# Kernel optimization log

Measured on AMD Instinct MI355X. Metric: run time of the kernel, lower is better.

## Reference

```python
import jax, jax.numpy as jnp
import numpy as np

B = 8388608  # batch

def moth(x, a, b):
    # per-feature parametric elementwise activation: a * x * sigmoid(b * x)
    return a * x * jax.nn.sigmoid(b * x)

def setup_inputs() -> dict:
    key = jax.random.key(0)
    ks = jax.random.split(key, 12)
    inp = {
        'x':  jax.random.normal(ks[0], (B, 2), dtype=jnp.float32),
        'W1': jax.random.normal(ks[1], (2, 8), dtype=jnp.float32) * (1.0 / np.sqrt(2)),
        'b1': jax.random.normal(ks[2], (8,), dtype=jnp.float32) * 0.01,
        'a1': jax.random.normal(ks[3], (8,), dtype=jnp.float32) * 0.1 + 1.0,
        'c1': jax.random.normal(ks[4], (8,), dtype=jnp.float32) * 0.1 + 1.0,
        'W2': jax.random.normal(ks[5], (8, 4), dtype=jnp.float32) * (1.0 / np.sqrt(8)),
        'b2': jax.random.normal(ks[6], (4,), dtype=jnp.float32) * 0.01,
        'a2': jax.random.normal(ks[7], (4,), dtype=jnp.float32) * 0.1 + 1.0,
        'c2': jax.random.normal(ks[8], (4,), dtype=jnp.float32) * 0.1 + 1.0,
        'W3': jax.random.normal(ks[9], (4, 1), dtype=jnp.float32) * (1.0 / np.sqrt(4)),
        'b3': jax.random.normal(ks[10], (1,), dtype=jnp.float32) * 0.01,
    }
    return inp

def reference(x, W1, b1, a1, c1, W2, b2, a2, c2, W3, b3):
    h = x @ W1 + b1            # [B, 8]
    h = moth(h, a1, c1)        # [B, 8]
    h = h @ W2 + b2            # [B, 4]
    h = moth(h, a2, c2)        # [B, 4]
    out = h @ W3 + b3          # [B, 1]
    return out
```

## Files before the change

kernel.cpp:

```cpp
#include <hip/hip_runtime.h>

#define NLOG2E -1.44269504088896340736f

typedef float f32x2 __attribute__((ext_vector_type(2)));


__global__ void prefold_kernel(
    const float* __restrict__ W1, const float* __restrict__ b1,
    const float* __restrict__ a1, const float* __restrict__ c1,
    const float* __restrict__ W2, const float* __restrict__ b2,
    const float* __restrict__ a2, const float* __restrict__ c2,
    const float* __restrict__ W3, const float* __restrict__ b3,
    float* __restrict__ C)
{
    if (threadIdx.x == 0 && blockIdx.x == 0) {
        for (int j = 0; j < 8; ++j) {
            float ncl = c1[j] * NLOG2E;
            C[j]      = W1[j]     * ncl;
            C[8 + j]  = W1[8 + j] * ncl;
            C[16 + j] = b1[j]     * ncl;
            float k1 = a1[j] / ncl;
            for (int k = 0; k < 4; ++k)
                C[24 + j * 4 + k] = W2[j * 4 + k] * k1;
        }
        for (int k = 0; k < 4; ++k) {
            C[56 + k] = b2[k];
            C[60 + k] = c2[k] * NLOG2E;
            C[64 + k] = a2[k] * W3[k];
        }
        C[68] = b3[0];
    }
}

__device__ __forceinline__ f32x2 moth2(float4 p, const f32x2* __restrict__ Cp,
                                       float bb3)
{
    f32x2 u[2][4];
#pragma unroll
    for (int r = 0; r < 2; ++r) {
        float X0 = r ? p.z : p.x;
        float X1 = r ? p.w : p.y;
        f32x2 x0b = {X0, X0};
        f32x2 x1b = {X1, X1};
#pragma unroll
        for (int pj = 0; pj < 4; ++pj)
            u[r][pj] = __builtin_elementwise_fma(
                           x0b, Cp[pj],
                           __builtin_elementwise_fma(x1b, Cp[4 + pj],
                                                     Cp[8 + pj]));
    }

#pragma unroll
    for (int r = 0; r < 2; ++r)
#pragma unroll
        for (int pj = 0; pj < 4; ++pj) {
            f32x2 e;
            e[0] = __builtin_amdgcn_exp2f(u[r][pj][0]);
            e[1] = __builtin_amdgcn_exp2f(u[r][pj][1]);
            f32x2 d = e + 1.0f;
            f32x2 s;
            s[0] = __builtin_amdgcn_rcpf(d[0]);
            s[1] = __builtin_amdgcn_rcpf(d[1]);
            u[r][pj] *= s;
        }

    f32x2 res;
#pragma unroll
    for (int r = 0; r < 2; ++r) {
        f32x2 ta = Cp[28], tb = Cp[29];
#pragma unroll
        for (int j = 0; j < 8; ++j) {
            float hj = u[r][j >> 1][j & 1];
            f32x2 hb = {hj, hj};
            ta = __builtin_elementwise_fma(hb, Cp[12 + j * 2 + 0], ta);
            tb = __builtin_elementwise_fma(hb, Cp[12 + j * 2 + 1], tb);
        }
        f32x2 u2a = Cp[30] * ta;
        f32x2 u2b = Cp[31] * tb;
        f32x2 ea, eb;
        ea[0] = __builtin_amdgcn_exp2f(u2a[0]);
        ea[1] = __builtin_amdgcn_exp2f(u2a[1]);
        eb[0] = __builtin_amdgcn_exp2f(u2b[0]);
        eb[1] = __builtin_amdgcn_exp2f(u2b[1]);
        f32x2 da = ea + 1.0f, db = eb + 1.0f;
        f32x2 sa, sb;
        sa[0] = __builtin_amdgcn_rcpf(da[0]);
        sa[1] = __builtin_amdgcn_rcpf(da[1]);
        sb[0] = __builtin_amdgcn_rcpf(db[0]);
        sb[1] = __builtin_amdgcn_rcpf(db[1]);
        f32x2 pa = ta * sa;
        f32x2 pb = tb * sb;
        f32x2 acc = {bb3, 0.0f};
        acc = __builtin_elementwise_fma(pa, Cp[32], acc);
        acc = __builtin_elementwise_fma(pb, Cp[33], acc);
        res[r] = acc[0] + acc[1];
    }
    return res;
}

__global__ __launch_bounds__(256, 6) void PlaygroundModel_66365834658304_kernel(
    const float* __restrict__ x, const float* __restrict__ C,
    float* __restrict__ out, int rows)
{
    const f32x2* Cp = (const f32x2*)C;
    float bb3 = C[68];

    long long n4f    = (long long)rows >> 1;
    long long g      = (long long)blockIdx.x * blockDim.x + threadIdx.x;
    long long stride = (long long)gridDim.x * blockDim.x;

    const float4* x4 = (const float4*)x;
    f32x2* o2 = (f32x2*)out;

    long long idx = g;
    if (idx < n4f) {
        float4 p = x4[idx];
        for (;;) {
            long long nidx = idx + stride;
            bool has = (nidx < n4f);
            float4 np;
            if (has) np = x4[nidx];
            o2[idx] = moth2(p, Cp, bb3);
            if (!has) break;
            p = np;
            idx = nidx;
        }
    }

    if (g == 0 && (rows & 1)) {
        const float* uw0  = C;
        const float* uw1  = C + 8;
        const float* ub   = C + 16;
        const float* w2f  = C + 24;
        const float* bb2  = C + 56;
        const float* ncl2 = C + 60;
        const float* aw2  = C + 64;
        long long rr = (long long)rows - 1;
        float x0 = x[rr * 2 + 0], x1 = x[rr * 2 + 1];
        float h[8];
#pragma unroll
        for (int j = 0; j < 8; ++j) {
            float uu = fmaf(x0, uw0[j], fmaf(x1, uw1[j], ub[j]));
            float s  = __builtin_amdgcn_rcpf(
                           1.0f + __builtin_amdgcn_exp2f(uu));
            h[j] = uu * s;
        }
        float o = bb3;
#pragma unroll
        for (int kk = 0; kk < 4; ++kk) {
            float t = bb2[kk];
#pragma unroll
            for (int j = 0; j < 8; ++j) t = fmaf(h[j], w2f[j * 4 + kk], t);
            float u2 = ncl2[kk] * t;
            float sg = __builtin_amdgcn_rcpf(
                           1.0f + __builtin_amdgcn_exp2f(u2));
            o = fmaf(t * sg, aw2[kk], o);
        }
        out[rr] = o;
    }
}

extern "C" void kernel_launch(void* const* d_in, const int* in_sizes, int n_in,
                              void* d_out, int out_size, void* d_ws, size_t ws_size,
                              hipStream_t stream) {
    const float* x  = (const float*)d_in[0];
    const float* W1 = (const float*)d_in[1];
    const float* b1 = (const float*)d_in[2];
    const float* a1 = (const float*)d_in[3];
    const float* c1 = (const float*)d_in[4];
    const float* W2 = (const float*)d_in[5];
    const float* b2 = (const float*)d_in[6];
    const float* a2 = (const float*)d_in[7];
    const float* c2 = (const float*)d_in[8];
    const float* W3 = (const float*)d_in[9];
    const float* b3 = (const float*)d_in[10];
    float* out = (float*)d_out;
    float* C   = (float*)d_ws;

    prefold_kernel<<<1, 64, 0, stream>>>(W1, b1, a1, c1, W2, b2, a2, c2,
                                         W3, b3, C);

    int rows = in_sizes[0] / 2;
    long long n4 = (long long)rows >> 1;

    int block = 256;
    long long want = (n4 + (long long)block * 4 - 1) / ((long long)block * 4);
    int grid = (int)(want < 1 ? 1 : (want > 4096 ? 4096 : want));

    PlaygroundModel_66365834658304_kernel<<<grid, block, 0, stream>>>(
        x, C, out, rows);
}
```

Measured before the change: 129.7 us.

## Deepen load prefetch to two iterations, use 32-bit indices, shrink grid

The grid-stride loop now keeps two float4 loads in flight ahead of compute, using clamped unconditional loads instead of a guarded single prefetch. Index arithmetic moves from 64-bit to 32-bit to cut scalar and address instructions. The grid is capped at 1536 blocks instead of 4096, so each thread runs more iterations. The clamped loads add a few redundant reads at the tail, and the smaller grid may lower occupancy and the latency hiding it provides.

```diff
diff --git a/kernel.cpp b/kernel.cpp
--- a/kernel.cpp
+++ b/kernel.cpp
@@ -105,25 +105,28 @@
     const f32x2* Cp = (const f32x2*)C;
     float bb3 = C[68];
 
-    long long n4f    = (long long)rows >> 1;
-    long long g      = (long long)blockIdx.x * blockDim.x + threadIdx.x;
-    long long stride = (long long)gridDim.x * blockDim.x;
+    int n4   = rows >> 1;
+    int n4m1 = n4 - 1;
+    int T    = (int)(gridDim.x * blockDim.x);
+    int g    = (int)(blockIdx.x * blockDim.x + threadIdx.x);
 
     const float4* x4 = (const float4*)x;
     f32x2* o2 = (f32x2*)out;
 
-    long long idx = g;
-    if (idx < n4f) {
-        float4 p = x4[idx];
-        for (;;) {
-            long long nidx = idx + stride;
-            bool has = (nidx < n4f);
-            float4 np;
-            if (has) np = x4[nidx];
-            o2[idx] = moth2(p, Cp, bb3);
-            if (!has) break;
-            p = np;
-            idx = nidx;
+    if (g < n4) {
+        int i0 = g;
+        int i1 = (i0 + T <= n4m1) ? i0 + T : n4m1;
+        float4 A = x4[i0];
+        float4 B = x4[i1];
+        int idx = i0, nxt = i0 + T;
+        while (true) {
+            int nn = nxt + T;
+            int ld = (nn <= n4m1) ? nn : n4m1;
+            float4 Cq = x4[ld];
+            o2[idx] = moth2(A, Cp, bb3);
+            if (nxt > n4m1) break;
+            A = B; B = Cq;
+            idx = nxt; nxt = nn;
         }
     }
 
@@ -135,8 +138,8 @@
         const float* bb2  = C + 56;
         const float* ncl2 = C + 60;
         const float* aw2  = C + 64;
-        long long rr = (long long)rows - 1;
-        float x0 = x[rr * 2 + 0], x1 = x[rr * 2 + 1];
+        int rr = rows - 1;
+        float x0 = x[(size_t)rr * 2 + 0], x1 = x[(size_t)rr * 2 + 1];
         float h[8];
 #pragma unroll
         for (int j = 0; j < 8; ++j) {
@@ -181,11 +184,13 @@
                                          W3, b3, C);
 
     int rows = in_sizes[0] / 2;
-    long long n4 = (long long)rows >> 1;
+    int n4   = rows >> 1;
 
     int block = 256;
-    long long want = (n4 + (long long)block * 4 - 1) / ((long long)block * 4);
-    int grid = (int)(want < 1 ? 1 : (want > 4096 ? 4096 : want));
+    int grid  = 1536;
+    int need  = (n4 + block - 1) / block;
+    if (need < grid) grid = need;
+    if (grid < 1) grid = 1;
 
     PlaygroundModel_66365834658304_kernel<<<grid, block, 0, stream>>>(
         x, C, out, rows);
```

Measured after the change: 129.2 us. About the same (-0.3%).
